# Kernel tuning notes

Hardware: AMD Instinct MI355X
Metric: run time of the kernel (lower is better)

## Reference

```python
import jax, jax.numpy as jnp
import numpy as np

D_MODEL = 1024
BATCH = 8
SEQ = 2048
LN_EPS = 1e-5


def setup_inputs() -> dict:
    key = jax.random.key(0)
    ks = jax.random.split(key, 8)
    scale = 0.1 / np.sqrt(D_MODEL)
    x = jax.random.normal(ks[0], (BATCH, SEQ, D_MODEL), dtype=jnp.float32)
    return {
        "x": x,
        "ln_w": jnp.ones((D_MODEL,), jnp.float32),
        "ln_b": jnp.zeros((D_MODEL,), jnp.float32),
        # layer_idx=0, n_layers=4 -> ratio_1 = 1.0 (init), perturb slightly for a non-trivial mix
        "tmk": jnp.ones((D_MODEL,), jnp.float32) * 0.9,
        "tmv": jnp.ones((D_MODEL,), jnp.float32) * 0.9,
        "tmr": jnp.ones((D_MODEL,), jnp.float32) * 0.9,
        "decay_w": jnp.full((D_MODEL,), -0.5, jnp.float32)
        + 0.1 * jax.random.normal(ks[1], (D_MODEL,), jnp.float32),
        "Wk": scale * jax.random.normal(ks[2], (D_MODEL, D_MODEL), jnp.float32),
        "Wv": scale * jax.random.normal(ks[3], (D_MODEL, D_MODEL), jnp.float32),
        "Wr": scale * jax.random.normal(ks[4], (D_MODEL, D_MODEL), jnp.float32),
        "Wo": scale * jax.random.normal(ks[5], (D_MODEL, D_MODEL), jnp.float32),
    }


def _layernorm(z, w, b):
    m = jnp.mean(z, axis=-1, keepdims=True)
    v = jnp.mean(jnp.square(z - m), axis=-1, keepdims=True)
    return (z - m) * jax.lax.rsqrt(v + LN_EPS) * w + b


def reference(x, ln_w, ln_b, tmk, tmv, tmr, decay_w, Wk, Wv, Wr, Wo):
    # x: (B, T, D)
    xn = _layernorm(x, ln_w, ln_b)
    # prev_x at t=0 is zeros (not LN of zeros), afterwards LN(x_{t-1})
    prev = jnp.pad(xn[:, :-1, :], ((0, 0), (1, 0), (0, 0)))
    xk = xn * tmk + prev * (1.0 - tmk)
    xv = xn * tmv + prev * (1.0 - tmv)
    xr = xn * tmr + prev * (1.0 - tmr)
    k = jnp.einsum("btd,ed->bte", xk, Wk)
    v = jnp.einsum("btd,ed->bte", xv, Wv)
    r = jax.nn.sigmoid(jnp.einsum("btd,ed->bte", xr, Wr))
    decay = jax.nn.sigmoid(decay_w)  # (D,)

    kv = (k * v).swapaxes(0, 1)  # (T, B, D) time-major for scan

    def step(S, kv_t):
        S_new = decay * S + kv_t
        return S_new, S_new

    S0 = jnp.zeros((x.shape[0], x.shape[2]), x.dtype)
    final_S, S_seq = jax.lax.scan(step, S0, kv)
    S_seq = S_seq.swapaxes(0, 1)  # (B, T, D)

    out = x + r * jnp.einsum("btd,ed->bte", S_seq, Wo)
    return out, final_S, S_seq
```

## Files before the change

### kernel.cpp

```cpp
#include <hip/hip_runtime.h>
#include <cstdint>

#define D_MODEL 1024
#define SEQ 2048
#define BATCH 8
#define M_TOTAL (BATCH*SEQ)
#define NC 64
#define CL (SEQ/NC)

typedef float f32x4 __attribute__((ext_vector_type(4)));
typedef short bf16x8 __attribute__((ext_vector_type(8)));
typedef unsigned short u16x4 __attribute__((ext_vector_type(4)));

__device__ __forceinline__ float b2f(unsigned short s){
  union { float f; unsigned u; } z; z.u = ((unsigned)s) << 16; return z.f;
}
__device__ __forceinline__ unsigned short f2b(float f){
  union { float f; unsigned u; } z; z.f = f;
  unsigned u = z.u;
  u += 0x7fffu + ((u >> 16) & 1u);
  return (unsigned short)(u >> 16);
}
__device__ __forceinline__ float sigmoidf_(float v){
  return 1.0f / (1.0f + __expf(-v));
}
__device__ __forceinline__ void gld_lds16(const void* g, void* l){
  __builtin_amdgcn_global_load_lds((const __attribute__((address_space(1))) unsigned int*)g,
                                   (__attribute__((address_space(3))) unsigned int*)l,
                                   16, 0, 0);
}

__device__ __forceinline__ void swz_mn(int bid, int& m0, int& n0){
  int xcd = bid & 7;
  int loc = bid >> 3;
  int wg  = xcd*64 + loc;
  m0 = (wg >> 3) * 256;
  n0 = (wg & 7) * 128;
}

__global__ __launch_bounds__(256) void wconv_kernel(const float* __restrict__ W0, const float* __restrict__ W1,
                                                    const float* __restrict__ W2, const float* __restrict__ W3,
                                                    unsigned short* __restrict__ WC){
  int mat = blockIdx.y;
  const float* src = (mat==0) ? W0 : (mat==1) ? W1 : (mat==2) ? W2 : W3;
  size_t i = ((size_t)blockIdx.x*256 + threadIdx.x)*4;
  f32x4 v = *(const f32x4*)(src + i);
  u16x4 o; o[0]=f2b(v[0]); o[1]=f2b(v[1]); o[2]=f2b(v[2]); o[3]=f2b(v[3]);
  *(u16x4*)(WC + (size_t)mat*1048576 + i) = o;
}

__global__ __launch_bounds__(256) void lnmix_kernel(const float* __restrict__ x,
                                                    const float* __restrict__ lnw, const float* __restrict__ lnb,
                                                    const float* __restrict__ tmk, const float* __restrict__ tmv,
                                                    const float* __restrict__ tmr,
                                                    unsigned short* __restrict__ XK, unsigned short* __restrict__ XV,
                                                    unsigned short* __restrict__ XR){
  int r0 = blockIdx.x * 8;
  int tid = threadIdx.x;
  bool seqfirst = (r0 & (SEQ-1)) == 0;
  size_t col = (size_t)tid*4;

  f32x4 xr[9];
  float s1[9], s2[9];
  #pragma unroll
  for (int i=0;i<9;i++){
    if (i==0 && seqfirst){
      xr[0][0]=0.f; xr[0][1]=0.f; xr[0][2]=0.f; xr[0][3]=0.f;
    } else {
      xr[i] = *(const f32x4*)(x + (size_t)(r0-1+i)*D_MODEL + col);
    }
    s1[i] = xr[i][0]+xr[i][1]+xr[i][2]+xr[i][3];
    s2[i] = xr[i][0]*xr[i][0]+xr[i][1]*xr[i][1]+xr[i][2]*xr[i][2]+xr[i][3]*xr[i][3];
  }
  #pragma unroll
  for (int off = 32; off > 0; off >>= 1){
    #pragma unroll
    for (int i=0;i<9;i++){
      s1[i] += __shfl_xor(s1[i], off);
      s2[i] += __shfl_xor(s2[i], off);
    }
  }
  __shared__ float red[4][18];
  int w = tid >> 6, lane = tid & 63;
  if (lane == 0){
    #pragma unroll
    for (int i=0;i<9;i++){ red[w][i]=s1[i]; red[w][9+i]=s2[i]; }
  }
  __syncthreads();
  float mean[9], rstd[9];
  #pragma unroll
  for (int i=0;i<9;i++){
    float a = red[0][i]+red[1][i]+red[2][i]+red[3][i];
    float b = red[0][9+i]+red[1][9+i]+red[2][9+i]+red[3][9+i];
    mean[i] = a*(1.0f/1024.0f);
    float var = b*(1.0f/1024.0f) - mean[i]*mean[i];
    rstd[i] = rsqrtf(var + 1e-5f);
  }

  f32x4 wv = *(const f32x4*)(lnw + col);
  f32x4 bv = *(const f32x4*)(lnb + col);
  f32x4 k4 = *(const f32x4*)(tmk + col);
  f32x4 v4 = *(const f32x4*)(tmv + col);
  f32x4 r4 = *(const f32x4*)(tmr + col);

  f32x4 np;
  if (seqfirst){ np[0]=0.f; np[1]=0.f; np[2]=0.f; np[3]=0.f; }
  else {
    #pragma unroll
    for (int j=0;j<4;j++) np[j] = (xr[0][j]-mean[0])*rstd[0]*wv[j] + bv[j];
  }
  #pragma unroll
  for (int i=0;i<8;i++){
    f32x4 nc;
    #pragma unroll
    for (int j=0;j<4;j++) nc[j] = (xr[i+1][j]-mean[i+1])*rstd[i+1]*wv[j] + bv[j];
    u16x4 ok, ov, orr;
    #pragma unroll
    for (int j=0;j<4;j++){
      ok[j]  = f2b(np[j] + k4[j]*(nc[j]-np[j]));
      ov[j]  = f2b(np[j] + v4[j]*(nc[j]-np[j]));
      orr[j] = f2b(np[j] + r4[j]*(nc[j]-np[j]));
    }
    size_t base = (size_t)(r0+i)*D_MODEL + col;
    *(u16x4*)(XK + base) = ok;
    *(u16x4*)(XV + base) = ov;
    *(u16x4*)(XR + base) = orr;
    np = nc;
  }
}

__device__ __forceinline__ void gemm256_core(const unsigned short* __restrict__ A,
                                             const unsigned short* __restrict__ W,
                                             int m0, int n0, int tid,
                                             unsigned short* As, unsigned short* Bs,
                                             f32x4 (&acc)[8][4]){
  int wid = tid >> 6, lane = tid & 63;
  int wm = wid >> 1, wn = wid & 1;
  int fr = lane & 15, fg = lane >> 4;

  int offAg[8], offBg[4];
  #pragma unroll
  for (int it = 0; it < 8; ++it){
    int chunk = it*256 + tid;
    int row = chunk >> 3;
    int cg = (chunk & 7) ^ (row & 7);
    offAg[it] = (m0+row)*D_MODEL + cg*8;
  }
  #pragma unroll
  for (int it = 0; it < 4; ++it){
    int chunk = it*256 + tid;
    int row = chunk >> 3;
    int cg = (chunk & 7) ^ (row & 7);
    offBg[it] = (n0+row)*D_MODEL + cg*8;
  }

  #define STAGE(kt_) { \
    _Pragma("unroll") \
    for (int it = 0; it < 8; ++it) \
      gld_lds16(A + offAg[it] + (kt_)*64, &As[(it*256+tid)*8]); \
    _Pragma("unroll") \
    for (int it = 0; it < 4; ++it) \
      gld_lds16(W + offBg[it] + (kt_)*64, &Bs[(it*256+tid)*8]); \
  }

  STAGE(0);

  bf16x8 aL[4][2], aH[4][2], bL[2][2], bH[2][2];

  #pragma unroll 1
  for (int kt = 0; kt < 16; ++kt){
    asm volatile("s_waitcnt vmcnt(0)" ::: "memory");
    __builtin_amdgcn_s_barrier();
    asm volatile("" ::: "memory");

    #pragma unroll
    for (int mi=0; mi<4; ++mi)
      #pragma unroll
      for (int ks=0; ks<2; ++ks){
        int r = wm*128 + mi*16 + fr;
        aL[mi][ks] = *(const bf16x8*)(&As[r*64 + (((ks*4+fg)^(r&7))<<3)]);
      }
    #pragma unroll
    for (int ni=0; ni<2; ++ni)
      #pragma unroll
      for (int ks=0; ks<2; ++ks){
        int r = wn*64 + ni*16 + fr;
        bL[ni][ks] = *(const bf16x8*)(&Bs[r*64 + (((ks*4+fg)^(r&7))<<3)]);
      }
    __builtin_amdgcn_s_barrier();
    asm volatile("s_waitcnt lgkmcnt(0)" ::: "memory");
    __builtin_amdgcn_s_setprio(1);
    #pragma unroll
    for (int mi=0; mi<4; ++mi)
      #pragma unroll
      for (int ni=0; ni<2; ++ni)
        #pragma unroll
        for (int ks=0; ks<2; ++ks)
          acc[mi][ni] = __builtin_amdgcn_mfma_f32_16x16x32_bf16(aL[mi][ks], bL[ni][ks], acc[mi][ni], 0, 0, 0);
    __builtin_amdgcn_s_setprio(0);
    __builtin_amdgcn_s_barrier();

    #pragma unroll
    for (int ni=0; ni<2; ++ni)
      #pragma unroll
      for (int ks=0; ks<2; ++ks){
        int r = wn*64 + (ni+2)*16 + fr;
        bH[ni][ks] = *(const bf16x8*)(&Bs[r*64 + (((ks*4+fg)^(r&7))<<3)]);
      }
    __builtin_amdgcn_s_barrier();
    asm volatile("s_waitcnt lgkmcnt(0)" ::: "memory");
    __builtin_amdgcn_s_setprio(1);
    #pragma unroll
    for (int mi=0; mi<4; ++mi)
      #pragma unroll
      for (int ni=0; ni<2; ++ni)
        #pragma unroll
        for (int ks=0; ks<2; ++ks)
          acc[mi][ni+2] = __builtin_amdgcn_mfma_f32_16x16x32_bf16(aL[mi][ks], bH[ni][ks], acc[mi][ni+2], 0, 0, 0);
    __builtin_amdgcn_s_setprio(0);
    __builtin_amdgcn_s_barrier();

    #pragma unroll
    for (int mi=0; mi<4; ++mi)
      #pragma unroll
      for (int ks=0; ks<2; ++ks){
        int r = wm*128 + (mi+4)*16 + fr;
        aH[mi][ks] = *(const bf16x8*)(&As[r*64 + (((ks*4+fg)^(r&7))<<3)]);
      }
    asm volatile("s_waitcnt lgkmcnt(0)" ::: "memory");
    __builtin_amdgcn_s_barrier();
    asm volatile("" ::: "memory");

    if (kt < 15) STAGE(kt+1);

    __builtin_amdgcn_s_setprio(1);
    #pragma unroll
    for (int mi=0; mi<4; ++mi)
      #pragma unroll
      for (int ni=0; ni<2; ++ni)
        #pragma unroll
        for (int ks=0; ks<2; ++ks)
          acc[mi+4][ni+2] = __builtin_amdgcn_mfma_f32_16x16x32_bf16(aH[mi][ks], bH[ni][ks], acc[mi+4][ni+2], 0, 0, 0);
    #pragma unroll
    for (int mi=0; mi<4; ++mi)
      #pragma unroll
      for (int ni=0; ni<2; ++ni)
        #pragma unroll
        for (int ks=0; ks<2; ++ks)
          acc[mi+4][ni] = __builtin_amdgcn_mfma_f32_16x16x32_bf16(aH[mi][ks], bL[ni][ks], acc[mi+4][ni], 0, 0, 0);
    __builtin_amdgcn_s_setprio(0);
  }
  #undef STAGE
}

__global__ __launch_bounds__(256, 2) void gemm_kr_kernel(const unsigned short* __restrict__ XK,
                                                         const unsigned short* __restrict__ XR,
                                                         const unsigned short* __restrict__ Wk,
                                                         const unsigned short* __restrict__ Wr,
                                                         unsigned short* __restrict__ KB,
                                                         unsigned short* __restrict__ RB){
  __shared__ alignas(16) unsigned short As[16384];
  __shared__ alignas(16) unsigned short Bs[8192];
  int m0, n0; swz_mn(blockIdx.x, m0, n0);
  int z = blockIdx.z;
  int tid = threadIdx.x;
  const unsigned short* A = z ? XR : XK;
  const unsigned short* W = z ? Wr : Wk;
  unsigned short* O       = z ? RB : KB;

  f32x4 acc[8][4];
  #pragma unroll
  for (int i=0;i<8;i++)
    #pragma unroll
    for (int j=0;j<4;j++){ acc[i][j][0]=0.f; acc[i][j][1]=0.f; acc[i][j][2]=0.f; acc[i][j][3]=0.f; }

  gemm256_core(A, W, m0, n0, tid, As, Bs, acc);

  int wid = tid >> 6, lane = tid & 63;
  int wm = wid >> 1, wn = wid & 1;
  int fr = lane & 15, fg = lane >> 4;
  #pragma unroll
  for (int mi=0; mi<8; ++mi){
    #pragma unroll
    for (int ni=0; ni<4; ++ni){
      int c = n0 + wn*64 + ni*16 + fr;
      #pragma unroll
      for (int j=0; j<4; ++j){
        int r = m0 + wm*128 + mi*16 + fg*4 + j;
        size_t idx = (size_t)r*D_MODEL + c;
        float val = acc[mi][ni][j];
        if (z) val = sigmoidf_(val);
        O[idx] = f2b(val);
      }
    }
  }
}

__global__ __launch_bounds__(256, 2) void gemm_v_kernel(const unsigned short* __restrict__ XV,
                                                        const unsigned short* __restrict__ Wv,
                                                        unsigned short* __restrict__ KB){
  __shared__ alignas(16) unsigned short As[16384];
  __shared__ alignas(16) unsigned short Bs[8192];
  int m0, n0; swz_mn(blockIdx.x, m0, n0);
  int tid = threadIdx.x;

  f32x4 acc[8][4];
  #pragma unroll
  for (int i=0;i<8;i++)
    #pragma unroll
    for (int j=0;j<4;j++){ acc[i][j][0]=0.f; acc[i][j][1]=0.f; acc[i][j][2]=0.f; acc[i][j][3]=0.f; }

  gemm256_core(XV, Wv, m0, n0, tid, As, Bs, acc);

  int wid = tid >> 6, lane = tid & 63;
  int wm = wid >> 1, wn = wid & 1;
  int fr = lane & 15, fg = lane >> 4;
  #pragma unroll
  for (int mi=0; mi<8; ++mi){
    #pragma unroll
    for (int ni=0; ni<4; ++ni){
      int c = n0 + wn*64 + ni*16 + fr;
      #pragma unroll
      for (int j=0; j<4; ++j){
        int r = m0 + wm*128 + mi*16 + fg*4 + j;
        size_t idx = (size_t)r*D_MODEL + c;
        KB[idx] = f2b(acc[mi][ni][j] * b2f(KB[idx]));
      }
    }
  }
}

__global__ __launch_bounds__(256, 2) void gemm_out_kernel(const unsigned short* __restrict__ Sb,
                                                          const unsigned short* __restrict__ Wo,
                                                          const float* __restrict__ x,
                                                          const unsigned short* __restrict__ RB,
                                                          float* __restrict__ out){
  __shared__ alignas(16) unsigned short As[16384];
  __shared__ alignas(16) unsigned short Bs[8192];
  int m0, n0; swz_mn(blockIdx.x, m0, n0);
  int tid = threadIdx.x;

  f32x4 acc[8][4];
  #pragma unroll
  for (int i=0;i<8;i++)
    #pragma unroll
    for (int j=0;j<4;j++){ acc[i][j][0]=0.f; acc[i][j][1]=0.f; acc[i][j][2]=0.f; acc[i][j][3]=0.f; }

  gemm256_core(Sb, Wo, m0, n0, tid, As, Bs, acc);

  int wid = tid >> 6, lane = tid & 63;
  int wm = wid >> 1, wn = wid & 1;
  int fr = lane & 15, fg = lane >> 4;
  #pragma unroll
  for (int mi=0; mi<8; ++mi){
    #pragma unroll
    for (int ni=0; ni<4; ++ni){
      int c = n0 + wn*64 + ni*16 + fr;
      #pragma unroll
      for (int j=0; j<4; ++j){
        int r = m0 + wm*128 + mi*16 + fg*4 + j;
        size_t idx = (size_t)r*D_MODEL + c;
        float rr = b2f(RB[idx]);
        out[idx] = x[idx] + rr * acc[mi][ni][j];
      }
    }
  }
}

__global__ __launch_bounds__(256) void scan_p1_kernel(const unsigned short* __restrict__ kv,
                                                      const float* __restrict__ dw,
                                                      float* __restrict__ carr){
  int bc = blockIdx.x;
  int b = bc >> 6, c = bc & (NC-1);
  int d0 = threadIdx.x * 4;
  float dx = sigmoidf_(dw[d0+0]);
  float dy = sigmoidf_(dw[d0+1]);
  float dz = sigmoidf_(dw[d0+2]);
  float dwv = sigmoidf_(dw[d0+3]);
  float Sx=0.f, Sy=0.f, Sz=0.f, Sw=0.f;
  size_t base = ((size_t)(b*SEQ + c*CL))*D_MODEL + d0;
  for (int i=0;i<CL;i++){
    u16x4 k4 = *(const u16x4*)(kv + base);
    Sx = dx*Sx + b2f(k4[0]);
    Sy = dy*Sy + b2f(k4[1]);
    Sz = dz*Sz + b2f(k4[2]);
    Sw = dwv*Sw + b2f(k4[3]);
    base += D_MODEL;
  }
  f32x4 o; o[0]=Sx; o[1]=Sy; o[2]=Sz; o[3]=Sw;
  *(f32x4*)(carr + (size_t)bc*D_MODEL + d0) = o;
}

__global__ __launch_bounds__(256) void scan_p2_kernel(const float* __restrict__ dw, float* __restrict__ carr){
  int gid = blockIdx.x*256 + threadIdx.x;
  int b = gid >> 10, d = gid & (D_MODEL-1);
  float dec = sigmoidf_(dw[d]);
  float dL = dec;
  #pragma unroll
  for (int i=0;i<5;i++) dL *= dL;
  float S = 0.f;
  for (int c=0;c<NC;c++){
    size_t idx = ((size_t)(b*NC + c))*D_MODEL + d;
    float cr = carr[idx];
    carr[idx] = S;
    S = dL*S + cr;
  }
}

__global__ __launch_bounds__(256) void scan_p3_kernel(const unsigned short* __restrict__ kv,
                                                      const float* __restrict__ dw,
                                                      const float* __restrict__ cin,
                                                      float* __restrict__ sseq,
                                                      float* __restrict__ finalS,
                                                      unsigned short* __restrict__ sb16){
  int bc = blockIdx.x;
  int b = bc >> 6, c = bc & (NC-1);
  int d0 = threadIdx.x * 4;
  float dx = sigmoidf_(dw[d0+0]);
  float dy = sigmoidf_(dw[d0+1]);
  float dz = sigmoidf_(dw[d0+2]);
  float dwv = sigmoidf_(dw[d0+3]);
  f32x4 S = *(const f32x4*)(cin + (size_t)bc*D_MODEL + d0);
  size_t base = ((size_t)(b*SEQ + c*CL))*D_MODEL + d0;
  for (int i=0;i<CL;i++){
    u16x4 k4 = *(const u16x4*)(kv + base);
    S[0] = dx*S[0] + b2f(k4[0]);
    S[1] = dy*S[1] + b2f(k4[1]);
    S[2] = dz*S[2] + b2f(k4[2]);
    S[3] = dwv*S[3] + b2f(k4[3]);
    *(f32x4*)(sseq + base) = S;
    u16x4 s4; s4[0]=f2b(S[0]); s4[1]=f2b(S[1]); s4[2]=f2b(S[2]); s4[3]=f2b(S[3]);
    *(u16x4*)(sb16 + base) = s4;
    base += D_MODEL;
  }
  if (c == NC-1)
    *(f32x4*)(finalS + (size_t)b*D_MODEL + d0) = S;
}

extern "C" void kernel_launch(void* const* d_in, const int* in_sizes, int n_in,
                              void* d_out, int out_size, void* d_ws, size_t ws_size,
                              hipStream_t stream){
  const float* x   = (const float*)d_in[0];
  const float* lnw = (const float*)d_in[1];
  const float* lnb = (const float*)d_in[2];
  const float* tmk = (const float*)d_in[3];
  const float* tmv = (const float*)d_in[4];
  const float* tmr = (const float*)d_in[5];
  const float* dw  = (const float*)d_in[6];
  const float* Wk  = (const float*)d_in[7];
  const float* Wv  = (const float*)d_in[8];
  const float* Wr  = (const float*)d_in[9];
  const float* Wo  = (const float*)d_in[10];

  float* out    = (float*)d_out;
  float* finalS = out + (size_t)M_TOTAL*D_MODEL;
  float* sseq   = finalS + (size_t)BATCH*D_MODEL;

  unsigned short* XK = (unsigned short*)d_out;
  unsigned short* XV = (unsigned short*)((char*)d_out + 33554432);
  unsigned short* XR = (unsigned short*)sseq;

  char* w = (char*)d_ws;
  unsigned short* WC   = (unsigned short*)(w + 0);
  unsigned short* SB16 = (unsigned short*)(w + 8388608);
  unsigned short* KB   = (unsigned short*)(w + 41943040);
  unsigned short* RB   = (unsigned short*)(w + 75497472);
  float*          CARR = (float*)(w + 109051904);

  wconv_kernel<<<dim3(1024,4), 256, 0, stream>>>(Wk, Wv, Wr, Wo, WC);
  lnmix_kernel<<<M_TOTAL/8, 256, 0, stream>>>(x, lnw, lnb, tmk, tmv, tmr, XK, XV, XR);

  gemm_kr_kernel<<<dim3(512,1,2), 256, 0, stream>>>(XK, XR, WC, WC + (size_t)2*1048576, KB, RB);
  gemm_v_kernel<<<512, 256, 0, stream>>>(XV, WC + (size_t)1048576, KB);

  scan_p1_kernel<<<BATCH*NC, 256, 0, stream>>>(KB, dw, CARR);
  scan_p2_kernel<<<32, 256, 0, stream>>>(dw, CARR);
  scan_p3_kernel<<<BATCH*NC, 256, 0, stream>>>(KB, dw, CARR, sseq, finalS, SB16);

  gemm_out_kernel<<<512, 256, 0, stream>>>(SB16, WC + (size_t)3*1048576, x, RB, out);
}
```

Before: 248.9 us.

## Double-buffer A tiles in LDS and load B operands directly from global

Restructures the GEMM core so B (weight) fragments are read straight from global memory into registers each k-step instead of going through LDS. A tiles are double-buffered in LDS, so the next tile's load overlaps the MFMA work, and the four-phase split with many barriers becomes one load-then-compute phase per step. This cuts barrier and LDS traffic but issues uncoalesced-ish direct global reads for B. It also doubles the A LDS footprint to 64KB and raises register pressure by holding all 8x2 A and 4x2 B fragments at once, which may hurt occupancy at 2 blocks per CU.

New measurement: 297.0 us. 1.19x slower.

```diff
diff --git a/kernel.cpp b/kernel.cpp
--- a/kernel.cpp
+++ b/kernel.cpp
@@ -129,16 +129,16 @@
   }
 }
 
-__device__ __forceinline__ void gemm256_core(const unsigned short* __restrict__ A,
-                                             const unsigned short* __restrict__ W,
-                                             int m0, int n0, int tid,
-                                             unsigned short* As, unsigned short* Bs,
-                                             f32x4 (&acc)[8][4]){
+__device__ __forceinline__ void gemm_core(const unsigned short* __restrict__ A,
+                                          const unsigned short* __restrict__ W,
+                                          int m0, int n0, int tid,
+                                          unsigned short* As,
+                                          f32x4 (&acc)[8][4]){
   int wid = tid >> 6, lane = tid & 63;
   int wm = wid >> 1, wn = wid & 1;
   int fr = lane & 15, fg = lane >> 4;
 
-  int offAg[8], offBg[4];
+  int offAg[8];
   #pragma unroll
   for (int it = 0; it < 8; ++it){
     int chunk = it*256 + tid;
@@ -146,111 +146,54 @@
     int cg = (chunk & 7) ^ (row & 7);
     offAg[it] = (m0+row)*D_MODEL + cg*8;
   }
-  #pragma unroll
-  for (int it = 0; it < 4; ++it){
-    int chunk = it*256 + tid;
-    int row = chunk >> 3;
-    int cg = (chunk & 7) ^ (row & 7);
-    offBg[it] = (n0+row)*D_MODEL + cg*8;
-  }
-
-  #define STAGE(kt_) { \
+  const unsigned short* Wb = W + (size_t)(n0 + wn*64 + fr)*D_MODEL + fg*8;
+
+  #define STAGEA(bsel, kt_) { \
     _Pragma("unroll") \
     for (int it = 0; it < 8; ++it) \
-      gld_lds16(A + offAg[it] + (kt_)*64, &As[(it*256+tid)*8]); \
-    _Pragma("unroll") \
-    for (int it = 0; it < 4; ++it) \
-      gld_lds16(W + offBg[it] + (kt_)*64, &Bs[(it*256+tid)*8]); \
-  }
-
-  STAGE(0);
-
-  bf16x8 aL[4][2], aH[4][2], bL[2][2], bH[2][2];
+      gld_lds16(A + offAg[it] + (kt_)*64, &As[(bsel)*16384 + (it*256+tid)*8]); }
+
+  STAGEA(0, 0);
+
+  bf16x8 a[8][2], b[4][2];
 
   #pragma unroll 1
   for (int kt = 0; kt < 16; ++kt){
-    asm volatile("s_waitcnt vmcnt(0)" ::: "memory");
+    const unsigned short* Ab = &As[(kt & 1)*16384];
+
+    #pragma unroll
+    for (int ni=0; ni<4; ++ni)
+      #pragma unroll
+      for (int ks=0; ks<2; ++ks)
+        b[ni][ks] = *(const bf16x8*)(Wb + (size_t)ni*16*D_MODEL + kt*64 + ks*32);
+
+    asm volatile("s_waitcnt vmcnt(8)" ::: "memory");
     __builtin_amdgcn_s_barrier();
-    asm volatile("" ::: "memory");
-
-    #pragma unroll
-    for (int mi=0; mi<4; ++mi)
+
+    #pragma unroll
+    for (int mi=0; mi<8; ++mi)
       #pragma unroll
       for (int ks=0; ks<2; ++ks){
         int r = wm*128 + mi*16 + fr;
-        aL[mi][ks] = *(const bf16x8*)(&As[r*64 + (((ks*4+fg)^(r&7))<<3)]);
+        a[mi][ks] = *(const bf16x8*)(&Ab[r*64 + (((ks*4+fg)^(r&7))<<3)]);
       }
-    #pragma unroll
-    for (int ni=0; ni<2; ++ni)
-      #pragma unroll
-      for (int ks=0; ks<2; ++ks){
-        int r = wn*64 + ni*16 + fr;
-        bL[ni][ks] = *(const bf16x8*)(&Bs[r*64 + (((ks*4+fg)^(r&7))<<3)]);
-      }
-    __builtin_amdgcn_s_barrier();
+
+    if (kt < 15) STAGEA((kt+1)&1, kt+1);
+
     asm volatile("s_waitcnt lgkmcnt(0)" ::: "memory");
+    __builtin_amdgcn_sched_barrier(0);
+
     __builtin_amdgcn_s_setprio(1);
     #pragma unroll
-    for (int mi=0; mi<4; ++mi)
-      #pragma unroll
-      for (int ni=0; ni<2; ++ni)
+    for (int mi=0; mi<8; ++mi)
+      #pragma unroll
+      for (int ni=0; ni<4; ++ni)
         #pragma unroll
         for (int ks=0; ks<2; ++ks)
-          acc[mi][ni] = __builtin_amdgcn_mfma_f32_16x16x32_bf16(aL[mi][ks], bL[ni][ks], acc[mi][ni], 0, 0, 0);
+          acc[mi][ni] = __builtin_amdgcn_mfma_f32_16x16x32_bf16(a[mi][ks], b[ni][ks], acc[mi][ni], 0, 0, 0);
     __builtin_amdgcn_s_setprio(0);
-    __builtin_amdgcn_s_barrier();
-
-    #pragma unroll
-    for (int ni=0; ni<2; ++ni)
-      #pragma unroll
-      for (int ks=0; ks<2; ++ks){
-        int r = wn*64 + (ni+2)*16 + fr;
-        bH[ni][ks] = *(const bf16x8*)(&Bs[r*64 + (((ks*4+fg)^(r&7))<<3)]);
-      }
-    __builtin_amdgcn_s_barrier();
-    asm volatile("s_waitcnt lgkmcnt(0)" ::: "memory");
-    __builtin_amdgcn_s_setprio(1);
-    #pragma unroll
-    for (int mi=0; mi<4; ++mi)
-      #pragma unroll
-      for (int ni=0; ni<2; ++ni)
-        #pragma unroll
-        for (int ks=0; ks<2; ++ks)
-          acc[mi][ni+2] = __builtin_amdgcn_mfma_f32_16x16x32_bf16(aL[mi][ks], bH[ni][ks], acc[mi][ni+2], 0, 0, 0);
-    __builtin_amdgcn_s_setprio(0);
-    __builtin_amdgcn_s_barrier();
-
-    #pragma unroll
-    for (int mi=0; mi<4; ++mi)
-      #pragma unroll
-      for (int ks=0; ks<2; ++ks){
-        int r = wm*128 + (mi+4)*16 + fr;
-        aH[mi][ks] = *(const bf16x8*)(&As[r*64 + (((ks*4+fg)^(r&7))<<3)]);
-      }
-    asm volatile("s_waitcnt lgkmcnt(0)" ::: "memory");
-    __builtin_amdgcn_s_barrier();
-    asm volatile("" ::: "memory");
-
-    if (kt < 15) STAGE(kt+1);
-
-    __builtin_amdgcn_s_setprio(1);
-    #pragma unroll
-    for (int mi=0; mi<4; ++mi)
-      #pragma unroll
-      for (int ni=0; ni<2; ++ni)
-        #pragma unroll
-        for (int ks=0; ks<2; ++ks)
-          acc[mi+4][ni+2] = __builtin_amdgcn_mfma_f32_16x16x32_bf16(aH[mi][ks], bH[ni][ks], acc[mi+4][ni+2], 0, 0, 0);
-    #pragma unroll
-    for (int mi=0; mi<4; ++mi)
-      #pragma unroll
-      for (int ni=0; ni<2; ++ni)
-        #pragma unroll
-        for (int ks=0; ks<2; ++ks)
-          acc[mi+4][ni] = __builtin_amdgcn_mfma_f32_16x16x32_bf16(aH[mi][ks], bL[ni][ks], acc[mi+4][ni], 0, 0, 0);
-    __builtin_amdgcn_s_setprio(0);
-  }
-  #undef STAGE
+  }
+  #undef STAGEA
 }
 
 __global__ __launch_bounds__(256, 2) void gemm_kr_kernel(const unsigned short* __restrict__ XK,
@@ -259,8 +202,7 @@
                                                          const unsigned short* __restrict__ Wr,
                                                          unsigned short* __restrict__ KB,
                                                          unsigned short* __restrict__ RB){
-  __shared__ alignas(16) unsigned short As[16384];
-  __shared__ alignas(16) unsigned short Bs[8192];
+  __shared__ alignas(16) unsigned short As[2*16384];
   int m0, n0; swz_mn(blockIdx.x, m0, n0);
   int z = blockIdx.z;
   int tid = threadIdx.x;
@@ -274,7 +216,7 @@
     #pragma unroll
     for (int j=0;j<4;j++){ acc[i][j][0]=0.f; acc[i][j][1]=0.f; acc[i][j][2]=0.f; acc[i][j][3]=0.f; }
 
-  gemm256_core(A, W, m0, n0, tid, As, Bs, acc);
+  gemm_core(A, W, m0, n0, tid, As, acc);
 
   int wid = tid >> 6, lane = tid & 63;
   int wm = wid >> 1, wn = wid & 1;
@@ -299,8 +241,7 @@
 __global__ __launch_bounds__(256, 2) void gemm_v_kernel(const unsigned short* __restrict__ XV,
                                                         const unsigned short* __restrict__ Wv,
                                                         unsigned short* __restrict__ KB){
-  __shared__ alignas(16) unsigned short As[16384];
-  __shared__ alignas(16) unsigned short Bs[8192];
+  __shared__ alignas(16) unsigned short As[2*16384];
   int m0, n0; swz_mn(blockIdx.x, m0, n0);
   int tid = threadIdx.x;
 
@@ -310,7 +251,7 @@
     #pragma unroll
     for (int j=0;j<4;j++){ acc[i][j][0]=0.f; acc[i][j][1]=0.f; acc[i][j][2]=0.f; acc[i][j][3]=0.f; }
 
-  gemm256_core(XV, Wv, m0, n0, tid, As, Bs, acc);
+  gemm_core(XV, Wv, m0, n0, tid, As, acc);
 
   int wid = tid >> 6, lane = tid & 63;
   int wm = wid >> 1, wn = wid & 1;
@@ -335,8 +276,7 @@
                                                           const float* __restrict__ x,
                                                           const unsigned short* __restrict__ RB,
                                                           float* __restrict__ out){
-  __shared__ alignas(16) unsigned short As[16384];
-  __shared__ alignas(16) unsigned short Bs[8192];
+  __shared__ alignas(16) unsigned short As[2*16384];
   int m0, n0; swz_mn(blockIdx.x, m0, n0);
   int tid = threadIdx.x;
 
@@ -346,7 +286,7 @@
     #pragma unroll
     for (int j=0;j<4;j++){ acc[i][j][0]=0.f; acc[i][j][1]=0.f; acc[i][j][2]=0.f; acc[i][j][3]=0.f; }
 
-  gemm256_core(Sb, Wo, m0, n0, tid, As, Bs, acc);
+  gemm_core(Sb, Wo, m0, n0, tid, As, acc);
 
   int wid = tid >> 6, lane = tid & 63;
   int wm = wid >> 1, wn = wid & 1;
```
